# Optimization experiments

Hardware: AMD Instinct MI355X
Metric: run time of the kernel (lower is better)

The kernel has to match this reference:

```python
import jax, jax.numpy as jnp
import numpy as np

B, N, H = 1, 512, 768  # batch, seq_len (incl. BOS/EOS), encoder_embed_dim


def setup_inputs() -> dict:
    key = jax.random.key(0)
    k1, k2 = jax.random.split(key, 2)
    inputs = jax.random.normal(k1, (B, N, H), dtype=jnp.float32)
    # Linear(2H -> 2): weight [2, 2H], bias [2]
    W = jax.random.normal(k2, (2, 2 * H), dtype=jnp.float32) * (1.0 / np.sqrt(2 * H)).astype(np.float32)
    b = jnp.zeros((2,), dtype=jnp.float32)
    return {"inputs": inputs, "W": W, "b": b}


def reference(inputs, W, b):
    # Pairwise features: prod and diff, each [B, N, N, H].
    # Linear on concat(prod, diff) == prod @ W1^T + diff @ W2^T (avoids materializing the concat).
    Hd = inputs.shape[-1]
    W1, W2 = W[:, :Hd], W[:, Hd:]
    prod = inputs[:, :, None, :] * inputs[:, None, :, :]
    diff = inputs[:, :, None, :] - inputs[:, None, :, :]
    pred = (jnp.einsum('bijh,oh->bijo', prod, W1)
            + jnp.einsum('bijh,oh->bijo', diff, W2)
            + b)  # [B, N, N, 2]
    # Symmetrize over the two sequence axes, then drop BOS/EOS positions.
    pred = (pred + pred.transpose(0, 2, 1, 3)) * 0.5
    return pred[:, 1:-1, 1:-1]  # [B, N-2, N-2, 2]
```

## Files before the change

kernel.cpp:

```cpp
#include <hip/hip_runtime.h>
#include <hip/hip_bf16.h>


constexpr int H   = 768;
constexpr int M   = 510;
constexpr int LDP = H + 8;

typedef __attribute__((ext_vector_type(8))) short short8;
typedef __attribute__((ext_vector_type(4))) float f32x4;

__device__ inline void cvt_store4(unsigned short* p, float4 v) {
  __hip_bfloat162 lo = __float22bfloat162_rn(make_float2(v.x, v.y));
  __hip_bfloat162 hi = __float22bfloat162_rn(make_float2(v.z, v.w));
  uint2 u;
  u.x = *(unsigned int*)&lo;
  u.y = *(unsigned int*)&hi;
  *(uint2*)p = u;
}

__device__ inline float4 mul4(float4 a, float4 b) {
  return make_float4(a.x * b.x, a.y * b.y, a.z * b.z, a.w * b.w);
}

__global__ __launch_bounds__(512, 1) void pairwise_head_mfma(
    const float* __restrict__ X, const float* __restrict__ W,
    const float* __restrict__ bias, float* __restrict__ out) {
  __shared__ __align__(16) unsigned short sm[3 * 32 * LDP];
  unsigned short* sA0 = sm;
  unsigned short* sA1 = sm + 32 * LDP;
  unsigned short* sB  = sm + 2 * 32 * LDP;

  const int tid = threadIdx.x;
  const int gi0 = blockIdx.y * 32;
  const int gj0 = blockIdx.x * 32;

  const int srow = tid >> 4;
  const int sc   = tid & 15;
  int arow = gi0 + 1 + srow; if (arow > 511) arow = 511;
  int brow = gj0 + 1 + srow; if (brow > 511) brow = 511;
  const float4* Xa = (const float4*)(X + (size_t)arow * H);
  const float4* Xb = (const float4*)(X + (size_t)brow * H);
  const float4* W0 = (const float4*)(W);
  const float4* W1 = (const float4*)(W + 1536);
  unsigned short* a0p = sA0 + srow * LDP + sc * 4;
  unsigned short* a1p = sA1 + srow * LDP + sc * 4;
  unsigned short* bp  = sB  + srow * LDP + sc * 4;

#pragma unroll
  for (int u = 0; u < 6; ++u) {
    const int cl = u * 32 + sc;
    float4 xa0 = Xa[cl], xa1 = Xa[cl + 16];
    float4 xb0 = Xb[cl], xb1 = Xb[cl + 16];
    float4 w00 = W0[cl], w01 = W0[cl + 16];
    float4 w10 = W1[cl], w11 = W1[cl + 16];
    cvt_store4(a0p + u * 128,      mul4(xa0, w00));
    cvt_store4(a0p + u * 128 + 64, mul4(xa1, w01));
    cvt_store4(a1p + u * 128,      mul4(xa0, w10));
    cvt_store4(a1p + u * 128 + 64, mul4(xa1, w11));
    cvt_store4(bp  + u * 128,      xb0);
    cvt_store4(bp  + u * 128 + 64, xb1);
  }
  __syncthreads();

  const int wave = tid >> 6;
  const int lane = tid & 63;
  const int lo = lane & 15;
  const int q  = lane >> 4;
  const int quad = wave & 3;
  const int kh   = wave >> 2;
  const int mi = quad >> 1;
  const int nj = quad & 1;
  const unsigned short* pa0 = sA0 + (mi * 16 + lo) * LDP + kh * 384 + q * 8;
  const unsigned short* pa1 = sA1 + (mi * 16 + lo) * LDP + kh * 384 + q * 8;
  const unsigned short* pb  = sB  + (nj * 16 + lo) * LDP + kh * 384 + q * 8;

  f32x4 acc0 = {0.f, 0.f, 0.f, 0.f};
  f32x4 acc1 = {0.f, 0.f, 0.f, 0.f};
#pragma unroll
  for (int c = 0; c < 12; ++c) {
    const short8 a0 = *(const short8*)(pa0 + c * 32);
    const short8 a1 = *(const short8*)(pa1 + c * 32);
    const short8 b  = *(const short8*)(pb  + c * 32);
    acc0 = __builtin_amdgcn_mfma_f32_16x16x32_bf16(a0, b, acc0, 0, 0, 0);
    acc1 = __builtin_amdgcn_mfma_f32_16x16x32_bf16(a1, b, acc1, 0, 0, 0);
  }

  __syncthreads();

  float* red = (float*)sm;
  if (kh == 1) {
#pragma unroll
    for (int r = 0; r < 4; ++r) {
      const int rl = q * 4 + r;
      float2 v = make_float2(acc0[r], acc1[r]);
      *(float2*)(red + ((quad * 16 + rl) * 17 + lo) * 2) = v;
    }
  }
  __syncthreads();

  if (kh == 0) {
    const float b0 = bias[0];
    const float b1 = bias[1];
    const int j  = gj0 + nj * 16 + lo;
    const int i0 = gi0 + mi * 16 + q * 4;
    if (j < M) {
#pragma unroll
      for (int r = 0; r < 4; ++r) {
        const int i = i0 + r;
        if (i < M) {
          const float2 p =
              *(const float2*)(red + ((quad * 16 + (q * 4 + r)) * 17 + lo) * 2);
          float2 v = make_float2(acc0[r] + p.x + b0, acc1[r] + p.y + b1);
          *(float2*)(out + ((size_t)i * M + j) * 2) = v;
        }
      }
    }
  }
}

extern "C" void kernel_launch(void* const* d_in, const int* in_sizes, int n_in,
                              void* d_out, int out_size, void* d_ws, size_t ws_size,
                              hipStream_t stream) {
  const float* X    = (const float*)d_in[0];
  const float* W    = (const float*)d_in[1];
  const float* bias = (const float*)d_in[2];
  float* out = (float*)d_out;

  dim3 grid(16, 16);
  dim3 block(512);
  hipLaunchKernelGGL(pairwise_head_mfma, grid, block, 0, stream,
                     X, W, bias, out);
}
```

Measured before the change: 62.18 us.

## Precompute bf16 operands in a prep kernel and read MFMA fragments from global

Adds a separate prep kernel that multiplies X by both weight halves, converts the results and X to bf16, and writes them to workspace once. The main kernel then loads MFMA fragments directly from global/L2 instead of staging them through LDS, which removes the per-block fp32 loading, conversion and LDS fill that was repeated for every tile. The K split goes from 2 to 4 waves-groups (1024 threads) with a three-way LDS reduction, and block IDs are remapped to improve L2 locality. It adds a second launch, and the uncoalesced global fragment reads depend on cache hits.

```diff
diff --git a/kernel.cpp b/kernel.cpp
--- a/kernel.cpp
+++ b/kernel.cpp
@@ -2,66 +2,57 @@
 #include <hip/hip_bf16.h>
 
 
-constexpr int H   = 768;
-constexpr int M   = 510;
-constexpr int LDP = H + 8;
+constexpr int H  = 768;
+constexpr int M  = 510;
+constexpr int NP = 512 * 768;
 
 typedef __attribute__((ext_vector_type(8))) short short8;
 typedef __attribute__((ext_vector_type(4))) float f32x4;
-
-__device__ inline void cvt_store4(unsigned short* p, float4 v) {
-  __hip_bfloat162 lo = __float22bfloat162_rn(make_float2(v.x, v.y));
-  __hip_bfloat162 hi = __float22bfloat162_rn(make_float2(v.z, v.w));
-  uint2 u;
-  u.x = *(unsigned int*)&lo;
-  u.y = *(unsigned int*)&hi;
-  *(uint2*)p = u;
-}
 
 __device__ inline float4 mul4(float4 a, float4 b) {
   return make_float4(a.x * b.x, a.y * b.y, a.z * b.z, a.w * b.w);
 }
 
-__global__ __launch_bounds__(512, 1) void pairwise_head_mfma(
+__device__ inline unsigned int cvt2(float a, float b) {
+  __hip_bfloat162 p = __float22bfloat162_rn(make_float2(a, b));
+  return *(unsigned int*)&p;
+}
+
+__device__ inline uint4 cvt8(float4 a, float4 b) {
+  uint4 u;
+  u.x = cvt2(a.x, a.y);
+  u.y = cvt2(a.z, a.w);
+  u.z = cvt2(b.x, b.y);
+  u.w = cvt2(b.z, b.w);
+  return u;
+}
+
+__global__ __launch_bounds__(256, 1) void prep_kernel(
     const float* __restrict__ X, const float* __restrict__ W,
-    const float* __restrict__ bias, float* __restrict__ out) {
-  __shared__ __align__(16) unsigned short sm[3 * 32 * LDP];
-  unsigned short* sA0 = sm;
-  unsigned short* sA1 = sm + 32 * LDP;
-  unsigned short* sB  = sm + 2 * 32 * LDP;
+    unsigned short* __restrict__ P) {
+  const int t  = blockIdx.x * 256 + threadIdx.x;
+  const int e0 = t * 8;
+  const int h  = e0 % H;
+  float4 x0  = *(const float4*)(X + e0);
+  float4 x1  = *(const float4*)(X + e0 + 4);
+  float4 w00 = *(const float4*)(W + h);
+  float4 w01 = *(const float4*)(W + h + 4);
+  float4 w10 = *(const float4*)(W + 1536 + h);
+  float4 w11 = *(const float4*)(W + 1536 + h + 4);
+  *(uint4*)(P + e0)          = cvt8(mul4(x0, w00), mul4(x1, w01));
+  *(uint4*)(P + NP + e0)     = cvt8(mul4(x0, w10), mul4(x1, w11));
+  *(uint4*)(P + 2 * NP + e0) = cvt8(x0, x1);
+}
 
-  const int tid = threadIdx.x;
-  const int gi0 = blockIdx.y * 32;
-  const int gj0 = blockIdx.x * 32;
+__global__ __launch_bounds__(1024, 1) void pairwise_head_mfma(
+    const unsigned short* __restrict__ P, const float* __restrict__ bias,
+    float* __restrict__ out) {
+  const int bid = blockIdx.x;
+  const int sb  = (bid & 7) * 32 + (bid >> 3);
+  const int gj0 = (sb & 15) * 32;
+  const int gi0 = (sb >> 4) * 32;
 
-  const int srow = tid >> 4;
-  const int sc   = tid & 15;
-  int arow = gi0 + 1 + srow; if (arow > 511) arow = 511;
-  int brow = gj0 + 1 + srow; if (brow > 511) brow = 511;
-  const float4* Xa = (const float4*)(X + (size_t)arow * H);
-  const float4* Xb = (const float4*)(X + (size_t)brow * H);
-  const float4* W0 = (const float4*)(W);
-  const float4* W1 = (const float4*)(W + 1536);
-  unsigned short* a0p = sA0 + srow * LDP + sc * 4;
-  unsigned short* a1p = sA1 + srow * LDP + sc * 4;
-  unsigned short* bp  = sB  + srow * LDP + sc * 4;
-
-#pragma unroll
-  for (int u = 0; u < 6; ++u) {
-    const int cl = u * 32 + sc;
-    float4 xa0 = Xa[cl], xa1 = Xa[cl + 16];
-    float4 xb0 = Xb[cl], xb1 = Xb[cl + 16];
-    float4 w00 = W0[cl], w01 = W0[cl + 16];
-    float4 w10 = W1[cl], w11 = W1[cl + 16];
-    cvt_store4(a0p + u * 128,      mul4(xa0, w00));
-    cvt_store4(a0p + u * 128 + 64, mul4(xa1, w01));
-    cvt_store4(a1p + u * 128,      mul4(xa0, w10));
-    cvt_store4(a1p + u * 128 + 64, mul4(xa1, w11));
-    cvt_store4(bp  + u * 128,      xb0);
-    cvt_store4(bp  + u * 128 + 64, xb1);
-  }
-  __syncthreads();
-
+  const int tid  = threadIdx.x;
   const int wave = tid >> 6;
   const int lane = tid & 63;
   const int lo = lane & 15;
@@ -70,14 +61,18 @@
   const int kh   = wave >> 2;
   const int mi = quad >> 1;
   const int nj = quad & 1;
-  const unsigned short* pa0 = sA0 + (mi * 16 + lo) * LDP + kh * 384 + q * 8;
-  const unsigned short* pa1 = sA1 + (mi * 16 + lo) * LDP + kh * 384 + q * 8;
-  const unsigned short* pb  = sB  + (nj * 16 + lo) * LDP + kh * 384 + q * 8;
+
+  int ar = gi0 + 1 + mi * 16 + lo; if (ar > 511) ar = 511;
+  int br = gj0 + 1 + nj * 16 + lo; if (br > 511) br = 511;
+  const int kb = kh * 192 + q * 8;
+  const unsigned short* pa0 = P          + ar * H + kb;
+  const unsigned short* pa1 = P + NP     + ar * H + kb;
+  const unsigned short* pb  = P + 2 * NP + br * H + kb;
 
   f32x4 acc0 = {0.f, 0.f, 0.f, 0.f};
   f32x4 acc1 = {0.f, 0.f, 0.f, 0.f};
 #pragma unroll
-  for (int c = 0; c < 12; ++c) {
+  for (int c = 0; c < 6; ++c) {
     const short8 a0 = *(const short8*)(pa0 + c * 32);
     const short8 a1 = *(const short8*)(pa1 + c * 32);
     const short8 b  = *(const short8*)(pb  + c * 32);
@@ -85,15 +80,12 @@
     acc1 = __builtin_amdgcn_mfma_f32_16x16x32_bf16(a1, b, acc1, 0, 0, 0);
   }
 
-  __syncthreads();
-
-  float* red = (float*)sm;
-  if (kh == 1) {
+  __shared__ __align__(16) float red[3 * 4 * 16 * 17 * 2];
+  if (kh > 0) {
 #pragma unroll
     for (int r = 0; r < 4; ++r) {
-      const int rl = q * 4 + r;
-      float2 v = make_float2(acc0[r], acc1[r]);
-      *(float2*)(red + ((quad * 16 + rl) * 17 + lo) * 2) = v;
+      const int idx = (((kh - 1) * 4 + quad) * 16 + q * 4 + r) * 17 + lo;
+      *(float2*)(red + idx * 2) = make_float2(acc0[r], acc1[r]);
     }
   }
   __syncthreads();
@@ -108,10 +100,16 @@
       for (int r = 0; r < 4; ++r) {
         const int i = i0 + r;
         if (i < M) {
-          const float2 p =
-              *(const float2*)(red + ((quad * 16 + (q * 4 + r)) * 17 + lo) * 2);
-          float2 v = make_float2(acc0[r] + p.x + b0, acc1[r] + p.y + b1);
-          *(float2*)(out + ((size_t)i * M + j) * 2) = v;
+          float s0 = acc0[r] + b0;
+          float s1 = acc1[r] + b1;
+#pragma unroll
+          for (int s = 0; s < 3; ++s) {
+            const int idx = ((s * 4 + quad) * 16 + q * 4 + r) * 17 + lo;
+            const float2 p = *(const float2*)(red + idx * 2);
+            s0 += p.x;
+            s1 += p.y;
+          }
+          *(float2*)(out + ((size_t)i * M + j) * 2) = make_float2(s0, s1);
         }
       }
     }
@@ -125,9 +123,9 @@
   const float* W    = (const float*)d_in[1];
   const float* bias = (const float*)d_in[2];
   float* out = (float*)d_out;
+  unsigned short* P = (unsigned short*)d_ws;
 
-  dim3 grid(16, 16);
-  dim3 block(512);
-  hipLaunchKernelGGL(pairwise_head_mfma, grid, block, 0, stream,
-                     X, W, bias, out);
+  hipLaunchKernelGGL(prep_kernel, dim3(192), dim3(256), 0, stream, X, W, P);
+  hipLaunchKernelGGL(pairwise_head_mfma, dim3(256), dim3(1024), 0, stream,
+                     P, bias, out);
 }
```

Result: slower. 68.79 us (+10.6%).

## Remap blocks per XCD for L2 locality and widen staging stores to 16 bytes

Applied to the files above, without the earlier changes.

Switches to a 1D grid and assigns tiles so that blocks landing on the same XCD (round-robin by block id) cover a compact 8x4 region of the output, improving L2 reuse of X rows. The shared-memory staging now loads two adjacent float4s per thread, batched three chunks at a time, and writes 16-byte bf16 vectors instead of 8-byte ones. Bias loads are hoisted to kernel start. Adds register pressure from the batched loads and assumes the XCD dispatch mapping.

```diff
diff --git a/kernel.cpp b/kernel.cpp
--- a/kernel.cpp
+++ b/kernel.cpp
@@ -9,17 +9,22 @@
 typedef __attribute__((ext_vector_type(8))) short short8;
 typedef __attribute__((ext_vector_type(4))) float f32x4;
 
-__device__ inline void cvt_store4(unsigned short* p, float4 v) {
-  __hip_bfloat162 lo = __float22bfloat162_rn(make_float2(v.x, v.y));
-  __hip_bfloat162 hi = __float22bfloat162_rn(make_float2(v.z, v.w));
-  uint2 u;
-  u.x = *(unsigned int*)&lo;
-  u.y = *(unsigned int*)&hi;
-  *(uint2*)p = u;
+__device__ inline float4 mul4(float4 a, float4 b) {
+  return make_float4(a.x * b.x, a.y * b.y, a.z * b.z, a.w * b.w);
 }
 
-__device__ inline float4 mul4(float4 a, float4 b) {
-  return make_float4(a.x * b.x, a.y * b.y, a.z * b.z, a.w * b.w);
+__device__ inline unsigned int cvt2(float a, float b) {
+  __hip_bfloat162 p = __float22bfloat162_rn(make_float2(a, b));
+  return *(unsigned int*)&p;
+}
+
+__device__ inline uint4 cvt8(float4 a, float4 b) {
+  uint4 u;
+  u.x = cvt2(a.x, a.y);
+  u.y = cvt2(a.z, a.w);
+  u.z = cvt2(b.x, b.y);
+  u.w = cvt2(b.z, b.w);
+  return u;
 }
 
 __global__ __launch_bounds__(512, 1) void pairwise_head_mfma(
@@ -30,9 +35,15 @@
   unsigned short* sA1 = sm + 32 * LDP;
   unsigned short* sB  = sm + 2 * 32 * LDP;
 
+  const int bid = blockIdx.x;
+  const int xcd = bid & 7;
+  const int k   = bid >> 3;
+  const int gi0 = ((xcd >> 1) * 4 + (k >> 3)) * 32;
+  const int gj0 = ((xcd & 1) * 8 + (k & 7)) * 32;
+
   const int tid = threadIdx.x;
-  const int gi0 = blockIdx.y * 32;
-  const int gj0 = blockIdx.x * 32;
+  const float b0 = bias[0];
+  const float b1 = bias[1];
 
   const int srow = tid >> 4;
   const int sc   = tid & 15;
@@ -42,23 +53,28 @@
   const float4* Xb = (const float4*)(X + (size_t)brow * H);
   const float4* W0 = (const float4*)(W);
   const float4* W1 = (const float4*)(W + 1536);
-  unsigned short* a0p = sA0 + srow * LDP + sc * 4;
-  unsigned short* a1p = sA1 + srow * LDP + sc * 4;
-  unsigned short* bp  = sB  + srow * LDP + sc * 4;
+  unsigned short* a0p = sA0 + srow * LDP + sc * 8;
+  unsigned short* a1p = sA1 + srow * LDP + sc * 8;
+  unsigned short* bp  = sB  + srow * LDP + sc * 8;
 
 #pragma unroll
-  for (int u = 0; u < 6; ++u) {
-    const int cl = u * 32 + sc;
-    float4 xa0 = Xa[cl], xa1 = Xa[cl + 16];
-    float4 xb0 = Xb[cl], xb1 = Xb[cl + 16];
-    float4 w00 = W0[cl], w01 = W0[cl + 16];
-    float4 w10 = W1[cl], w11 = W1[cl + 16];
-    cvt_store4(a0p + u * 128,      mul4(xa0, w00));
-    cvt_store4(a0p + u * 128 + 64, mul4(xa1, w01));
-    cvt_store4(a1p + u * 128,      mul4(xa0, w10));
-    cvt_store4(a1p + u * 128 + 64, mul4(xa1, w11));
-    cvt_store4(bp  + u * 128,      xb0);
-    cvt_store4(bp  + u * 128 + 64, xb1);
+  for (int hf = 0; hf < 2; ++hf) {
+    float4 r[3][8];
+#pragma unroll
+    for (int v = 0; v < 3; ++v) {
+      const int c2 = (hf * 3 + v) * 32 + sc * 2;
+      r[v][0] = Xa[c2]; r[v][1] = Xa[c2 + 1];
+      r[v][2] = Xb[c2]; r[v][3] = Xb[c2 + 1];
+      r[v][4] = W0[c2]; r[v][5] = W0[c2 + 1];
+      r[v][6] = W1[c2]; r[v][7] = W1[c2 + 1];
+    }
+#pragma unroll
+    for (int v = 0; v < 3; ++v) {
+      const int off = (hf * 3 + v) * 128;
+      *(uint4*)(a0p + off) = cvt8(mul4(r[v][0], r[v][4]), mul4(r[v][1], r[v][5]));
+      *(uint4*)(a1p + off) = cvt8(mul4(r[v][0], r[v][6]), mul4(r[v][1], r[v][7]));
+      *(uint4*)(bp  + off) = cvt8(r[v][2], r[v][3]);
+    }
   }
   __syncthreads();
 
@@ -99,8 +115,6 @@
   __syncthreads();
 
   if (kh == 0) {
-    const float b0 = bias[0];
-    const float b1 = bias[1];
     const int j  = gj0 + nj * 16 + lo;
     const int i0 = gi0 + mi * 16 + q * 4;
     if (j < M) {
@@ -126,7 +140,7 @@
   const float* bias = (const float*)d_in[2];
   float* out = (float*)d_out;
 
-  dim3 grid(16, 16);
+  dim3 grid(256);
   dim3 block(512);
   hipLaunchKernelGGL(pairwise_head_mfma, grid, block, 0, stream,
                      X, W, bias, out);
```

After: 62.22 us. Within noise of the previous version (+0.1%).
